# Kernel tuning notes

Hardware: AMD Instinct MI355X
Metric: run time of the kernel (lower is better)

Reference implementation:

```python
import jax, jax.numpy as jnp
import numpy as np

N = 50000
E = 1600000

def setup_inputs() -> dict:
    key = jax.random.key(0)
    ks = jax.random.split(key, 8)
    x = jax.random.normal(ks[0], (N, 512), dtype=jnp.float32)
    edge_index = jax.random.randint(ks[1], (2, E), 0, N, dtype=jnp.int32).astype(jnp.int64)
    eigenvectors = jax.random.normal(ks[2], (N, 128), dtype=jnp.float32)
    W1 = jax.random.normal(ks[3], (512, 128), dtype=jnp.float32) * 0.04
    b1 = jnp.zeros((128,), dtype=jnp.float32)
    W2 = jax.random.normal(ks[4], (128, 64), dtype=jnp.float32) * 0.09
    b2 = jnp.zeros((64,), dtype=jnp.float32)
    lin_W = jax.random.normal(ks[5], (128, 64), dtype=jnp.float32) * 0.09
    W3 = jax.random.normal(ks[6], (128, 40), dtype=jnp.float32) * 0.09
    b3 = jnp.zeros((40,), dtype=jnp.float32)
    return {"x": x, "edge_index": edge_index, "eigenvectors": eigenvectors,
            "W1": W1, "b1": b1, "W2": W2, "b2": b2, "lin_W": lin_W, "W3": W3, "b3": b3}

def _gcn_norm(edge_index, num_nodes):
    # add self loops, then symmetric normalization D^-1/2 (A+I) D^-1/2
    loop = jnp.arange(num_nodes, dtype=edge_index.dtype)
    row = jnp.concatenate([edge_index[0], loop])  # source
    col = jnp.concatenate([edge_index[1], loop])  # target
    w = jnp.ones(row.shape[0], dtype=jnp.float32)
    deg = jax.ops.segment_sum(w, col, num_segments=num_nodes)
    dis = jnp.where(deg > 0, 1.0 / jnp.sqrt(deg), 0.0)
    norm = dis[row] * dis[col]  # [E+N]
    return row, col, norm

def _gcn_conv(h, W, b, row, col, norm, num_nodes):
    h = h @ W                                  # [N, d_out] linear first (PyG order)
    msg = h[row] * norm[:, None]               # gather + scale, [E+N, d_out]
    out = jax.ops.segment_sum(msg, col, num_segments=num_nodes)  # scatter-add
    return out + b

def reference(x, edge_index, eigenvectors, W1, b1, W2, b2, lin_W, W3, b3):
    num_nodes = x.shape[0]
    row, col, norm = _gcn_norm(edge_index, num_nodes)
    h = jax.nn.relu(_gcn_conv(x, W1, b1, row, col, norm, num_nodes))
    # dropout omitted: eval mode (deterministic reference)
    h = jax.nn.relu(_gcn_conv(h, W2, b2, row, col, norm, num_nodes))
    xp = eigenvectors @ lin_W                  # Linear(spec_in, spec_out, bias=False)
    h = jnp.concatenate([h, xp], axis=1)       # [N, h2+spec_out]
    h = _gcn_conv(h, W3, b3, row, col, norm, num_nodes)
    return jax.nn.log_softmax(h, axis=1)
```

## Files before the change

### kernel.cpp

```cpp
#include <hip/hip_runtime.h>
#include <cstdint>
#include <cstddef>

constexpr int BLK = 256;
constexpr int NB = 128;

static inline size_t ws_align(size_t x) { return (x + 255) & ~size_t(255); }

typedef __attribute__((ext_vector_type(8))) short bf16x8;
typedef __attribute__((ext_vector_type(4))) float f32x4;

__device__ inline unsigned short f2bf(float f) {
  unsigned int u = __float_as_uint(f);
  unsigned int r = (u + 0x7fffu + ((u >> 16) & 1u)) >> 16;
  return (unsigned short)r;
}
__device__ inline float bf2f(unsigned short u) {
  return __uint_as_float(((unsigned int)u) << 16);
}
__device__ inline float bf2f_lo(unsigned int w) {
  return __uint_as_float(w << 16);
}
__device__ inline float bf2f_hi(unsigned int w) {
  return __uint_as_float(w & 0xffff0000u);
}

__device__ inline void gload16(const void* gp, void* lp) {
  __builtin_amdgcn_global_load_lds(
      (const __attribute__((address_space(1))) void*)gp,
      (__attribute__((address_space(3))) void*)lp, 16, 0, 0);
}

__global__ void k_pack_wt(const int* __restrict__ ei, unsigned int* __restrict__ pk,
                          int* __restrict__ cnt, int E, int nChunk,
                          const float* __restrict__ W1, const float* __restrict__ W2,
                          const float* __restrict__ linW, const float* __restrict__ W3,
                          unsigned short* __restrict__ WT1, unsigned short* __restrict__ WT2,
                          unsigned short* __restrict__ WTl, unsigned short* __restrict__ WT3) {
  if (blockIdx.x >= NB) {
    int i = (blockIdx.x - NB) * BLK + threadIdx.x;
    if (i < 65536) {
      int n = i >> 9, kg = i & 511;
      int tile = kg >> 5, k = kg & 31;
      WT1[tile * 4096 + n * 32 + k] = f2bf(W1[(size_t)kg * 128 + n]);
    } else if (i < 73728) {
      int j = i - 65536; int n = j >> 7, k = j & 127;
      WT2[j] = f2bf(W2[(size_t)k * 64 + n]);
    } else if (i < 81920) {
      int j = i - 73728; int n = j >> 7, k = j & 127;
      WTl[j] = f2bf(linW[(size_t)k * 64 + n]);
    } else if (i < 88064) {
      int j = i - 81920; int n = j >> 7, k = j & 127;
      WT3[j] = f2bf(n < 40 ? W3[(size_t)k * 40 + n] : 0.f);
    }
    return;
  }
  __shared__ int hist[256];
  for (int t = threadIdx.x; t < 256; t += BLK) hist[t] = 0;
  __syncthreads();
  int allz = 1;
  #pragma unroll 8
  for (int i = 0; i < 32; ++i) allz &= (ei[2 * i + 1] == 0) ? 1 : 0;
  const bool i64 = allz != 0;
  int beg = blockIdx.x * nChunk, end = min(beg + nChunk, E);
  for (int i = beg + threadIdx.x; i < end; i += BLK) {
    int row, col;
    if (i64) { row = ei[2 * i]; col = ei[2 * (E + i)]; }
    else     { row = ei[i];     col = ei[E + i]; }
    unsigned int p = ((unsigned int)col << 16) | (unsigned int)row;
    pk[i] = p;
    atomicAdd(&hist[col >> 8], 1);
  }
  __syncthreads();
  for (int t = threadIdx.x; t < 256; t += BLK) cnt[blockIdx.x * 256 + t] = hist[t];
}

__global__ void k_wscan(const int* __restrict__ cnt, int* __restrict__ woffs,
                        int* __restrict__ base, int nb, int E) {
  __shared__ int wsums[5];
  int w = threadIdx.x;
  int s = 0;
  for (int b = 0; b < nb; ++b) s += cnt[b * 256 + w];
  int lane = w & 63, wv = w >> 6;
  int x = s;
  #pragma unroll
  for (int sh = 1; sh < 64; sh <<= 1) { int t = __shfl_up(x, sh); if (lane >= sh) x += t; }
  if (lane == 63) wsums[wv] = x;
  __syncthreads();
  if (w == 0) { int a = 0; for (int k = 0; k < 4; ++k) { int t = wsums[k]; wsums[k] = a; a += t; } }
  __syncthreads();
  int excl = x - s + wsums[wv];
  woffs[w] = excl;
  if (w == 255) woffs[256] = excl + s;
  int start = excl;
  for (int b = 0; b < nb; ++b) { base[b * 256 + w] = start; start += cnt[b * 256 + w]; }
}

__global__ __launch_bounds__(256)
void k_part_gemm1(const unsigned int* __restrict__ pk, const int* __restrict__ base,
                  unsigned int* __restrict__ P, int E, int nChunk,
                  const float* __restrict__ x, const unsigned short* __restrict__ WT,
                  unsigned short* __restrict__ C, int N, int gG1) {
  __shared__ __align__(16) char smem[49152];
  if ((int)blockIdx.x >= gG1) {
    const int pb = (int)blockIdx.x - gG1;
    int* cur = (int*)smem;
    for (int t = threadIdx.x; t < 256; t += BLK) cur[t] = base[pb * 256 + t];
    __syncthreads();
    int beg = pb * nChunk, end = min(beg + nChunk, E);
    for (int i = beg + threadIdx.x; i < end; i += BLK) {
      unsigned int p = pk[i];
      int pos = atomicAdd(&cur[p >> 24], 1);
      P[pos] = p;
    }
    return;
  }
  float* As0 = (float*)smem;
  unsigned short* Wsl0 = (unsigned short*)(smem + 24576);
  const int tid = threadIdx.x;
  const int lane = tid & 63, wv = tid >> 6;
  const int m = lane & 15, kq = lane >> 4;
  const int row0 = (int)blockIdx.x * 64;

  const int r8 = lane >> 3;
  const int c8 = lane & 7;
  int agrow[2];
  #pragma unroll
  for (int jj = 0; jj < 2; ++jj) {
    int gr = row0 + wv * 16 + jj * 8 + r8;
    agrow[jj] = gr < N ? gr : N - 1;
  }

  f32x4 acc[8];
  #pragma unroll
  for (int t = 0; t < 8; ++t) acc[t] = {0.f, 0.f, 0.f, 0.f};

  auto STAGE = [&](int pb, int kb) {
    #pragma unroll
    for (int jj = 0; jj < 2; ++jj) {
      const float* src = x + (size_t)agrow[jj] * 512 + kb * 32 + (c8 ^ r8) * 4;
      gload16(src, As0 + pb * 2048 + (wv * 16 + jj * 8) * 32);
    }
    #pragma unroll
    for (int jj = 0; jj < 2; ++jj) {
      const unsigned short* src = WT + (size_t)kb * 4096 + wv * 1024 + jj * 512;
      gload16(src, Wsl0 + pb * 4096 + wv * 1024 + jj * 512);
    }
  };

  STAGE(0, 0);
  int cur = 0;
  #pragma unroll 1
  for (int t = 0; t < 16; ++t) {
    int nxt = cur + 1; if (nxt == 3) nxt = 0;
    if (t < 15) {
      STAGE(nxt, t + 1);
      asm volatile("s_waitcnt vmcnt(4)" ::: "memory");
    } else {
      asm volatile("s_waitcnt vmcnt(0)" ::: "memory");
    }
    __builtin_amdgcn_s_barrier();
    __builtin_amdgcn_sched_barrier(0);

    const char* Ab = (const char*)(As0 + cur * 2048);
    const char* Wb = (const char*)(Wsl0 + cur * 4096);
    const int row = wv * 16 + m;
    const int s = row & 7;
    f32x4 lo = *(const f32x4*)(Ab + row * 128 + ((kq * 2) ^ s) * 16);
    f32x4 hi = *(const f32x4*)(Ab + row * 128 + ((kq * 2 + 1) ^ s) * 16);
    bf16x8 af;
    af[0] = (short)f2bf(lo[0]); af[1] = (short)f2bf(lo[1]);
    af[2] = (short)f2bf(lo[2]); af[3] = (short)f2bf(lo[3]);
    af[4] = (short)f2bf(hi[0]); af[5] = (short)f2bf(hi[1]);
    af[6] = (short)f2bf(hi[2]); af[7] = (short)f2bf(hi[3]);
    #pragma unroll
    for (int tt = 0; tt < 8; ++tt) {
      int wrow = tt * 16 + m;
      bf16x8 bf = *(const bf16x8*)(Wb + wrow * 64 + kq * 16);
      acc[tt] = __builtin_amdgcn_mfma_f32_16x16x32_bf16(af, bf, acc[tt], 0, 0, 0);
    }
    cur = nxt;
  }

  #pragma unroll
  for (int r = 0; r < 4; ++r) {
    int rr = row0 + wv * 16 + kq * 4 + r;
    if (rr < N) {
      #pragma unroll
      for (int t = 0; t < 8; ++t)
        C[(size_t)rr * 128 + t * 16 + m] = f2bf(acc[t][r]);
    }
  }
}

__global__ void k_window_build(const unsigned int* __restrict__ P,
                               const int* __restrict__ woffs,
                               float* __restrict__ dis, int* __restrict__ offs,
                               int* __restrict__ csr, int N, int E) {
  __shared__ int hist[256];
  __shared__ int wsums[5];
  __shared__ int lbase[256];
  const int node0 = blockIdx.x * 256;
  const int t = threadIdx.x;
  hist[t] = 0;
  __syncthreads();
  const int beg = woffs[blockIdx.x], end = woffs[blockIdx.x + 1];
  for (int i = beg + t; i < end; i += BLK)
    atomicAdd(&hist[(P[i] >> 16) & 255], 1);
  __syncthreads();
  const int dg = hist[t];
  if (node0 + t < N) dis[node0 + t] = 1.0f / sqrtf((float)(dg + 1));
  int lane = t & 63, wv = t >> 6;
  int x = dg;
  #pragma unroll
  for (int sh = 1; sh < 64; sh <<= 1) { int q = __shfl_up(x, sh); if (lane >= sh) x += q; }
  if (lane == 63) wsums[wv] = x;
  __syncthreads();
  if (t == 0) { int a = 0; for (int k = 0; k < 4; ++k) { int q = wsums[k]; wsums[k] = a; a += q; } }
  __syncthreads();
  const int goff = beg + (x - dg + wsums[wv]);
  if (node0 + t < N) offs[node0 + t] = goff;
  lbase[t] = goff;
  __syncthreads();
  for (int i = beg + t; i < end; i += BLK) {
    unsigned int p = P[i];
    int pos = atomicAdd(&lbase[(p >> 16) & 255], 1);
    csr[pos] = (int)(p & 0xffffu);
  }
  if (blockIdx.x == 0 && t == 0) offs[N] = E;
}

template<int NT, int MR, bool AF32>
__device__ inline void mgemm_body(int bi, const void* __restrict__ Av,
                                  const unsigned short* __restrict__ WT,
                                  const float* __restrict__ dis, unsigned short* __restrict__ C,
                                  int ldc, int NOUT, int N) {
  constexpr int K = 128;
  const int tid = threadIdx.x;
  const int lane = tid & 63;
  const int wv = tid >> 6;
  const int m = lane & 15;
  const int kq = lane >> 4;
  const int orow = bi * (64 * MR) + wv * (16 * MR);

  int rowc[MR];
  #pragma unroll
  for (int mr = 0; mr < MR; ++mr) {
    int row = orow + mr * 16 + m;
    rowc[mr] = row < N ? row : N - 1;
  }

  f32x4 acc[MR][NT];
  #pragma unroll
  for (int mr = 0; mr < MR; ++mr)
    #pragma unroll
    for (int t = 0; t < NT; ++t) acc[mr][t] = {0.f, 0.f, 0.f, 0.f};

  #pragma unroll 4
  for (int k0 = 0; k0 < K; k0 += 32) {
    bf16x8 af[MR];
    #pragma unroll
    for (int mr = 0; mr < MR; ++mr) {
      if constexpr (AF32) {
        const float* Arow = (const float*)Av + (size_t)rowc[mr] * K + kq * 8 + k0;
        float4 a0 = *(const float4*)Arow;
        float4 a1 = *(const float4*)(Arow + 4);
        af[mr][0] = (short)f2bf(a0.x); af[mr][1] = (short)f2bf(a0.y);
        af[mr][2] = (short)f2bf(a0.z); af[mr][3] = (short)f2bf(a0.w);
        af[mr][4] = (short)f2bf(a1.x); af[mr][5] = (short)f2bf(a1.y);
        af[mr][6] = (short)f2bf(a1.z); af[mr][7] = (short)f2bf(a1.w);
      } else {
        const unsigned short* Arow = (const unsigned short*)Av + (size_t)rowc[mr] * K + kq * 8 + k0;
        af[mr] = *(const bf16x8*)Arow;
      }
    }
    bf16x8 bf[NT];
    #pragma unroll
    for (int t = 0; t < NT; ++t)
      bf[t] = *(const bf16x8*)(WT + (size_t)(t * 16 + m) * K + k0 + kq * 8);
    #pragma unroll
    for (int t = 0; t < NT; ++t)
      #pragma unroll
      for (int mr = 0; mr < MR; ++mr)
        acc[mr][t] = __builtin_amdgcn_mfma_f32_16x16x32_bf16(af[mr], bf[t], acc[mr][t], 0, 0, 0);
  }
  #pragma unroll
  for (int mr = 0; mr < MR; ++mr) {
    #pragma unroll
    for (int r = 0; r < 4; ++r) {
      int rr = orow + mr * 16 + kq * 4 + r;
      if (rr < N) {
        float s = dis ? dis[rr] : 1.f;
        #pragma unroll
        for (int t = 0; t < NT; ++t) {
          int cc = t * 16 + m;
          if (cc < NOUT)
            C[(size_t)rr * ldc + cc] = f2bf(acc[mr][t][r] * s);
        }
      }
    }
  }
}

__global__ __launch_bounds__(256)
void k_mgemm2x(const unsigned short* __restrict__ G, const unsigned short* __restrict__ WT2,
               const float* __restrict__ dis, unsigned short* __restrict__ F,
               const float* __restrict__ eig, const unsigned short* __restrict__ WTl,
               unsigned short* __restrict__ XP, int N, int nA) {
  if ((int)blockIdx.x < nA)
    mgemm_body<4, 2, false>(blockIdx.x, G, WT2, dis, F, 64, 64, N);
  else
    mgemm_body<4, 2, true>(blockIdx.x - nA, eig, WTl, nullptr, XP, 64, 64, N);
}

__global__ __launch_bounds__(256)
void k_mgemm3(const unsigned short* __restrict__ H2, const unsigned short* __restrict__ XP,
              const unsigned short* __restrict__ WT3, const float* __restrict__ dis,
              unsigned short* __restrict__ C, int N) {
  constexpr int NT = 3, MR = 2;
  const int tid = threadIdx.x;
  const int lane = tid & 63;
  const int wv = tid >> 6;
  const int m = lane & 15;
  const int kq = lane >> 4;
  const int orow = blockIdx.x * (64 * MR) + wv * (16 * MR);

  int rowc[MR];
  #pragma unroll
  for (int mr = 0; mr < MR; ++mr) {
    int row = orow + mr * 16 + m;
    rowc[mr] = row < N ? row : N - 1;
  }

  f32x4 acc[MR][NT];
  #pragma unroll
  for (int mr = 0; mr < MR; ++mr)
    #pragma unroll
    for (int t = 0; t < NT; ++t) acc[mr][t] = {0.f, 0.f, 0.f, 0.f};

  #pragma unroll 4
  for (int k0 = 0; k0 < 128; k0 += 32) {
    const unsigned short* Abase = (k0 < 64) ? H2 : XP;
    const int kk = (k0 & 63) + kq * 8;
    bf16x8 af[MR];
    #pragma unroll
    for (int mr = 0; mr < MR; ++mr)
      af[mr] = *(const bf16x8*)(Abase + (size_t)rowc[mr] * 64 + kk);
    bf16x8 bf[NT];
    #pragma unroll
    for (int t = 0; t < NT; ++t)
      bf[t] = *(const bf16x8*)(WT3 + (size_t)(t * 16 + m) * 128 + k0 + kq * 8);
    #pragma unroll
    for (int t = 0; t < NT; ++t)
      #pragma unroll
      for (int mr = 0; mr < MR; ++mr)
        acc[mr][t] = __builtin_amdgcn_mfma_f32_16x16x32_bf16(af[mr], bf[t], acc[mr][t], 0, 0, 0);
  }
  #pragma unroll
  for (int mr = 0; mr < MR; ++mr) {
    #pragma unroll
    for (int r = 0; r < 4; ++r) {
      int rr = orow + mr * 16 + kq * 4 + r;
      if (rr < N) {
        float s = dis[rr];
        #pragma unroll
        for (int t = 0; t < NT; ++t) {
          int cc = t * 16 + m;
          if (cc < 40)
            C[(size_t)rr * 40 + cc] = f2bf(acc[mr][t][r] * s);
        }
      }
    }
  }
}

template<int D, bool RELU, bool GDIS>
__launch_bounds__(BLK)
__global__ void k_agg2(const unsigned short* __restrict__ g, int ldg,
                       const float* __restrict__ dis, const float* __restrict__ bias,
                       const int* __restrict__ offs, const int* __restrict__ csr,
                       unsigned short* __restrict__ dst, int ldd, int N) {
  constexpr int CPL = D / 32;
  int wid = (blockIdx.x * BLK + threadIdx.x) >> 6;
  int lane = threadIdx.x & 63;
  if (wid >= N) return;
  const int l5 = lane >> 5, c = lane & 31;
  const float dv = dis[wid];
  float acc[CPL];
  #pragma unroll
  for (int k = 0; k < CPL; ++k) acc[k] = 0.f;

  auto addrow = [&](int r, float w) {
    if constexpr (CPL == 4) {
      uint2 v = *(const uint2*)&g[(size_t)r * ldg + c * 4];
      acc[0] = fmaf(w, bf2f_lo(v.x), acc[0]); acc[1] = fmaf(w, bf2f_hi(v.x), acc[1]);
      acc[2] = fmaf(w, bf2f_lo(v.y), acc[2]); acc[3] = fmaf(w, bf2f_hi(v.y), acc[3]);
    } else {
      unsigned int v = *(const unsigned int*)&g[(size_t)r * ldg + c * 2];
      acc[0] = fmaf(w, bf2f_lo(v), acc[0]); acc[1] = fmaf(w, bf2f_hi(v), acc[1]);
    }
  };

  if (l5 == 0) addrow(wid, GDIS ? dv : 1.0f);
  int beg = offs[wid], end = offs[wid + 1];
  for (int e0 = beg; e0 < end; e0 += 64) {
    int cnt = end - e0; if (cnt > 64) cnt = 64;
    int u = (lane < cnt) ? csr[e0 + lane] : 0;
    float du = 1.0f;
    if constexpr (GDIS) du = (lane < cnt) ? dis[u] : 0.f;
    int j = 0;
    for (; j + 3 < cnt; j += 4) {
      int r0 = __shfl(u, j + l5);
      int r1 = __shfl(u, j + 2 + l5);
      float w0 = GDIS ? __shfl(du, j + l5) : 1.0f;
      float w1 = GDIS ? __shfl(du, j + 2 + l5) : 1.0f;
      addrow(r0, w0); addrow(r1, w1);
    }
    for (; j < cnt; j += 2) {
      int jj = j + l5;
      int si = jj < cnt ? jj : j;
      int r0 = __shfl(u, si);
      float w0 = GDIS ? __shfl(du, si) : 1.0f;
      if (jj < cnt) addrow(r0, w0);
    }
  }
  #pragma unroll
  for (int k = 0; k < CPL; ++k) acc[k] += __shfl_xor(acc[k], 32);

  if (l5 == 0) {
    float o[CPL];
    #pragma unroll
    for (int k = 0; k < CPL; ++k) {
      o[k] = dv * acc[k] + bias[c * CPL + k];
      if constexpr (RELU) o[k] = fmaxf(o[k], 0.f);
    }
    if constexpr (CPL == 4) {
      uint2 pw;
      pw.x = (unsigned)f2bf(o[0]) | ((unsigned)f2bf(o[1]) << 16);
      pw.y = (unsigned)f2bf(o[2]) | ((unsigned)f2bf(o[3]) << 16);
      *(uint2*)&dst[(size_t)wid * ldd + c * 4] = pw;
    } else {
      unsigned int pw = (unsigned)f2bf(o[0]) | ((unsigned)f2bf(o[1]) << 16);
      *(unsigned int*)&dst[(size_t)wid * ldd + c * 2] = pw;
    }
  }
}

__launch_bounds__(BLK)
__global__ void k_agg40(const unsigned short* __restrict__ g,
                        const float* __restrict__ dis, const float* __restrict__ bias,
                        const int* __restrict__ offs, const int* __restrict__ csr,
                        float* __restrict__ dst, int N) {
  int wid = (blockIdx.x * BLK + threadIdx.x) >> 6;
  int lane = threadIdx.x & 63;
  if (wid >= N) return;
  const int l5 = lane >> 5, c = lane & 31;
  const bool act = c < 20;
  float a0 = 0.f, a1 = 0.f;
  auto addrow = [&](int r) {
    if (act) {
      unsigned int w = *(const unsigned int*)&g[(size_t)r * 40 + c * 2];
      a0 += bf2f_lo(w); a1 += bf2f_hi(w);
    }
  };
  if (l5 == 0) addrow(wid);
  int beg = offs[wid], end = offs[wid + 1];
  for (int e0 = beg; e0 < end; e0 += 64) {
    int cnt = end - e0; if (cnt > 64) cnt = 64;
    int u = (lane < cnt) ? csr[e0 + lane] : 0;
    int j = 0;
    for (; j + 3 < cnt; j += 4) {
      int r0 = __shfl(u, j + l5);
      int r1 = __shfl(u, j + 2 + l5);
      addrow(r0); addrow(r1);
    }
    for (; j < cnt; j += 2) {
      int jj = j + l5;
      int r0 = __shfl(u, jj < cnt ? jj : j);
      if (jj < cnt) addrow(r0);
    }
  }
  a0 += __shfl_xor(a0, 32);
  a1 += __shfl_xor(a1, 32);

  if (l5 == 0) {
    float dv = dis[wid];
    float o0 = act ? dv * a0 + bias[c * 2]     : -__builtin_inff();
    float o1 = act ? dv * a1 + bias[c * 2 + 1] : -__builtin_inff();
    float mx = fmaxf(o0, o1);
    #pragma unroll
    for (int s = 16; s >= 1; s >>= 1) mx = fmaxf(mx, __shfl_down(mx, s, 32));
    mx = __shfl(mx, 0, 32);
    float ex = act ? (expf(o0 - mx) + expf(o1 - mx)) : 0.f;
    #pragma unroll
    for (int s = 16; s >= 1; s >>= 1) ex += __shfl_down(ex, s, 32);
    float ls = logf(__shfl(ex, 0, 32));
    if (act) {
      float2 r = make_float2(o0 - mx - ls, o1 - mx - ls);
      *(float2*)&dst[(size_t)wid * 40 + c * 2] = r;
    }
  }
}

extern "C" void kernel_launch(void* const* d_in, const int* in_sizes, int n_in,
                              void* d_out, int out_size, void* d_ws, size_t ws_size,
                              hipStream_t stream) {
  const float* x    = (const float*)d_in[0];
  const int*   ei   = (const int*)d_in[1];
  const float* eig  = (const float*)d_in[2];
  const float* W1   = (const float*)d_in[3];
  const float* b1   = (const float*)d_in[4];
  const float* W2   = (const float*)d_in[5];
  const float* b2   = (const float*)d_in[6];
  const float* linW = (const float*)d_in[7];
  const float* W3   = (const float*)d_in[8];
  const float* b3   = (const float*)d_in[9];
  float* out = (float*)d_out;

  const int N = in_sizes[0] / 512;
  const int E = in_sizes[1] / 2;

  char* ws = (char*)d_ws;
  size_t off = 0;
  auto alloc = [&](size_t bytes) { char* p = ws + off; off = ws_align(off + bytes); return p; };
  unsigned int* pk = (unsigned int*)alloc((size_t)E * 4);
  unsigned int* P  = (unsigned int*)alloc((size_t)E * 4);
  int*   csr    = (int*)alloc((size_t)E * 4);
  int*   offs   = (int*)alloc((size_t)(N + 1) * 4);
  int*   cnt    = (int*)alloc((size_t)NB * 256 * 4);
  int*   base   = (int*)alloc((size_t)NB * 256 * 4);
  int*   woffs  = (int*)alloc(257 * 4);
  float* dis    = (float*)alloc((size_t)N * 4);
  unsigned short* F  = (unsigned short*)alloc((size_t)N * 128 * 2);
  unsigned short* G  = (unsigned short*)alloc((size_t)N * 128 * 2);
  unsigned short* XP = (unsigned short*)alloc((size_t)N * 64 * 2);
  unsigned short* H2 = (unsigned short*)alloc((size_t)N * 64 * 2);
  unsigned short* WT1 = (unsigned short*)alloc(128 * 512 * 2);
  unsigned short* WT2 = (unsigned short*)alloc(64 * 128 * 2);
  unsigned short* WTl = (unsigned short*)alloc(64 * 128 * 2);
  unsigned short* WT3 = (unsigned short*)alloc(48 * 128 * 2);

  const int nChunk = (E + NB - 1) / NB;
  const int NW = (N + 255) / 256;
  const int WTB = (88064 + BLK - 1) / BLK;
  const int gG1 = (N + 63) / 64;
  const int gA = (N + 3) / 4;

  k_pack_wt<<<NB + WTB, BLK, 0, stream>>>(ei, pk, cnt, E, nChunk,
                                          W1, W2, linW, W3, WT1, WT2, WTl, WT3);
  k_wscan<<<1, 256, 0, stream>>>(cnt, woffs, base, NB, E);
  k_part_gemm1<<<gG1 + NB, BLK, 0, stream>>>(pk, base, P, E, nChunk, x, WT1, F, N, gG1);
  k_window_build<<<NW, BLK, 0, stream>>>(P, woffs, dis, offs, csr, N, E);

  k_agg2<128, true, true><<<gA, BLK, 0, stream>>>(F, 128, dis, b1, offs, csr, G, 128, N);
  k_mgemm2x<<<2 * ((N + 127) / 128), BLK, 0, stream>>>(G, WT2, dis, F, eig, WTl, XP, N, (N + 127) / 128);
  k_agg2<64, true, false><<<gA, BLK, 0, stream>>>(F, 64, dis, b2, offs, csr, H2, 64, N);
  k_mgemm3<<<(N + 127) / 128, BLK, 0, stream>>>(H2, XP, WT3, dis, F, N);
  k_agg40<<<gA, BLK, 0, stream>>>(F, dis, b3, offs, csr, out, N);
}
```

Measured before the change: 286.8 us.

## Fold spectral linear into W3 and fuse layer-3 GEMM into layer-2 aggregation

Precomputes the product linW·W3[64:] so the eigenvector branch maps straight to 40 outputs, and computes that projection inside the gemm1/partition launch. The layer-2 aggregation kernel now also applies ReLU and multiplies by the top half of W3 in registers, then adds the precomputed spectral term. This removes the separate mgemm3 launch and the H2/XP round trips through memory. In exchange the aggregation kernel does extra shuffle-based matvec work per node, and the weights are folded in a different order, which changes rounding.

After: 348.8 us. 1.22x slower.

```diff
diff --git a/kernel.cpp b/kernel.cpp
--- a/kernel.cpp
+++ b/kernel.cpp
@@ -34,9 +34,9 @@
 __global__ void k_pack_wt(const int* __restrict__ ei, unsigned int* __restrict__ pk,
                           int* __restrict__ cnt, int E, int nChunk,
                           const float* __restrict__ W1, const float* __restrict__ W2,
-                          const float* __restrict__ linW, const float* __restrict__ W3,
+                          const float* __restrict__ W3,
                           unsigned short* __restrict__ WT1, unsigned short* __restrict__ WT2,
-                          unsigned short* __restrict__ WTl, unsigned short* __restrict__ WT3) {
+                          unsigned short* __restrict__ W3aT) {
   if (blockIdx.x >= NB) {
     int i = (blockIdx.x - NB) * BLK + threadIdx.x;
     if (i < 65536) {
@@ -46,12 +46,9 @@
     } else if (i < 73728) {
       int j = i - 65536; int n = j >> 7, k = j & 127;
       WT2[j] = f2bf(W2[(size_t)k * 64 + n]);
-    } else if (i < 81920) {
-      int j = i - 73728; int n = j >> 7, k = j & 127;
-      WTl[j] = f2bf(linW[(size_t)k * 64 + n]);
-    } else if (i < 88064) {
-      int j = i - 81920; int n = j >> 7, k = j & 127;
-      WT3[j] = f2bf(n < 40 ? W3[(size_t)k * 40 + n] : 0.f);
+    } else if (i < 76288) {
+      int j2 = i - 73728; int jj = j2 >> 6, k = j2 & 63;
+      W3aT[j2] = f2bf(W3[(size_t)k * 40 + jj]);
     }
     return;
   }
@@ -75,8 +72,25 @@
   for (int t = threadIdx.x; t < 256; t += BLK) cnt[blockIdx.x * 256 + t] = hist[t];
 }
 
-__global__ void k_wscan(const int* __restrict__ cnt, int* __restrict__ woffs,
-                        int* __restrict__ base, int nb, int E) {
+__global__ void k_wscan_w3c(const int* __restrict__ cnt, int* __restrict__ woffs,
+                            int* __restrict__ base, int nb, int E,
+                            const float* __restrict__ linW, const float* __restrict__ W3,
+                            unsigned short* __restrict__ WT3c) {
+  if (blockIdx.x > 0) {
+    int jbase = ((int)blockIdx.x - 1) * 12;
+    for (int idx = threadIdx.x; idx < 12 * 128; idx += BLK) {
+      int j = jbase + (idx >> 7), k = idx & 127;
+      if (j >= 48) continue;
+      float v = 0.f;
+      if (j < 40) {
+        const float* lrow = linW + (size_t)k * 64;
+        #pragma unroll 8
+        for (int t = 0; t < 64; ++t) v += lrow[t] * W3[(size_t)(64 + t) * 40 + j];
+      }
+      WT3c[(size_t)j * 128 + k] = f2bf(v);
+    }
+    return;
+  }
   __shared__ int wsums[5];
   int w = threadIdx.x;
   int s = 0;
@@ -94,140 +108,6 @@
   if (w == 255) woffs[256] = excl + s;
   int start = excl;
   for (int b = 0; b < nb; ++b) { base[b * 256 + w] = start; start += cnt[b * 256 + w]; }
-}
-
-__global__ __launch_bounds__(256)
-void k_part_gemm1(const unsigned int* __restrict__ pk, const int* __restrict__ base,
-                  unsigned int* __restrict__ P, int E, int nChunk,
-                  const float* __restrict__ x, const unsigned short* __restrict__ WT,
-                  unsigned short* __restrict__ C, int N, int gG1) {
-  __shared__ __align__(16) char smem[49152];
-  if ((int)blockIdx.x >= gG1) {
-    const int pb = (int)blockIdx.x - gG1;
-    int* cur = (int*)smem;
-    for (int t = threadIdx.x; t < 256; t += BLK) cur[t] = base[pb * 256 + t];
-    __syncthreads();
-    int beg = pb * nChunk, end = min(beg + nChunk, E);
-    for (int i = beg + threadIdx.x; i < end; i += BLK) {
-      unsigned int p = pk[i];
-      int pos = atomicAdd(&cur[p >> 24], 1);
-      P[pos] = p;
-    }
-    return;
-  }
-  float* As0 = (float*)smem;
-  unsigned short* Wsl0 = (unsigned short*)(smem + 24576);
-  const int tid = threadIdx.x;
-  const int lane = tid & 63, wv = tid >> 6;
-  const int m = lane & 15, kq = lane >> 4;
-  const int row0 = (int)blockIdx.x * 64;
-
-  const int r8 = lane >> 3;
-  const int c8 = lane & 7;
-  int agrow[2];
-  #pragma unroll
-  for (int jj = 0; jj < 2; ++jj) {
-    int gr = row0 + wv * 16 + jj * 8 + r8;
-    agrow[jj] = gr < N ? gr : N - 1;
-  }
-
-  f32x4 acc[8];
-  #pragma unroll
-  for (int t = 0; t < 8; ++t) acc[t] = {0.f, 0.f, 0.f, 0.f};
-
-  auto STAGE = [&](int pb, int kb) {
-    #pragma unroll
-    for (int jj = 0; jj < 2; ++jj) {
-      const float* src = x + (size_t)agrow[jj] * 512 + kb * 32 + (c8 ^ r8) * 4;
-      gload16(src, As0 + pb * 2048 + (wv * 16 + jj * 8) * 32);
-    }
-    #pragma unroll
-    for (int jj = 0; jj < 2; ++jj) {
-      const unsigned short* src = WT + (size_t)kb * 4096 + wv * 1024 + jj * 512;
-      gload16(src, Wsl0 + pb * 4096 + wv * 1024 + jj * 512);
-    }
-  };
-
-  STAGE(0, 0);
-  int cur = 0;
-  #pragma unroll 1
-  for (int t = 0; t < 16; ++t) {
-    int nxt = cur + 1; if (nxt == 3) nxt = 0;
-    if (t < 15) {
-      STAGE(nxt, t + 1);
-      asm volatile("s_waitcnt vmcnt(4)" ::: "memory");
-    } else {
-      asm volatile("s_waitcnt vmcnt(0)" ::: "memory");
-    }
-    __builtin_amdgcn_s_barrier();
-    __builtin_amdgcn_sched_barrier(0);
-
-    const char* Ab = (const char*)(As0 + cur * 2048);
-    const char* Wb = (const char*)(Wsl0 + cur * 4096);
-    const int row = wv * 16 + m;
-    const int s = row & 7;
-    f32x4 lo = *(const f32x4*)(Ab + row * 128 + ((kq * 2) ^ s) * 16);
-    f32x4 hi = *(const f32x4*)(Ab + row * 128 + ((kq * 2 + 1) ^ s) * 16);
-    bf16x8 af;
-    af[0] = (short)f2bf(lo[0]); af[1] = (short)f2bf(lo[1]);
-    af[2] = (short)f2bf(lo[2]); af[3] = (short)f2bf(lo[3]);
-    af[4] = (short)f2bf(hi[0]); af[5] = (short)f2bf(hi[1]);
-    af[6] = (short)f2bf(hi[2]); af[7] = (short)f2bf(hi[3]);
-    #pragma unroll
-    for (int tt = 0; tt < 8; ++tt) {
-      int wrow = tt * 16 + m;
-      bf16x8 bf = *(const bf16x8*)(Wb + wrow * 64 + kq * 16);
-      acc[tt] = __builtin_amdgcn_mfma_f32_16x16x32_bf16(af, bf, acc[tt], 0, 0, 0);
-    }
-    cur = nxt;
-  }
-
-  #pragma unroll
-  for (int r = 0; r < 4; ++r) {
-    int rr = row0 + wv * 16 + kq * 4 + r;
-    if (rr < N) {
-      #pragma unroll
-      for (int t = 0; t < 8; ++t)
-        C[(size_t)rr * 128 + t * 16 + m] = f2bf(acc[t][r]);
-    }
-  }
-}
-
-__global__ void k_window_build(const unsigned int* __restrict__ P,
-                               const int* __restrict__ woffs,
-                               float* __restrict__ dis, int* __restrict__ offs,
-                               int* __restrict__ csr, int N, int E) {
-  __shared__ int hist[256];
-  __shared__ int wsums[5];
-  __shared__ int lbase[256];
-  const int node0 = blockIdx.x * 256;
-  const int t = threadIdx.x;
-  hist[t] = 0;
-  __syncthreads();
-  const int beg = woffs[blockIdx.x], end = woffs[blockIdx.x + 1];
-  for (int i = beg + t; i < end; i += BLK)
-    atomicAdd(&hist[(P[i] >> 16) & 255], 1);
-  __syncthreads();
-  const int dg = hist[t];
-  if (node0 + t < N) dis[node0 + t] = 1.0f / sqrtf((float)(dg + 1));
-  int lane = t & 63, wv = t >> 6;
-  int x = dg;
-  #pragma unroll
-  for (int sh = 1; sh < 64; sh <<= 1) { int q = __shfl_up(x, sh); if (lane >= sh) x += q; }
-  if (lane == 63) wsums[wv] = x;
-  __syncthreads();
-  if (t == 0) { int a = 0; for (int k = 0; k < 4; ++k) { int q = wsums[k]; wsums[k] = a; a += q; } }
-  __syncthreads();
-  const int goff = beg + (x - dg + wsums[wv]);
-  if (node0 + t < N) offs[node0 + t] = goff;
-  lbase[t] = goff;
-  __syncthreads();
-  for (int i = beg + t; i < end; i += BLK) {
-    unsigned int p = P[i];
-    int pos = atomicAdd(&lbase[(p >> 16) & 255], 1);
-    csr[pos] = (int)(p & 0xffffu);
-  }
-  if (blockIdx.x == 0 && t == 0) offs[N] = E;
 }
 
 template<int NT, int MR, bool AF32>
@@ -303,75 +183,149 @@
 }
 
 __global__ __launch_bounds__(256)
-void k_mgemm2x(const unsigned short* __restrict__ G, const unsigned short* __restrict__ WT2,
-               const float* __restrict__ dis, unsigned short* __restrict__ F,
-               const float* __restrict__ eig, const unsigned short* __restrict__ WTl,
-               unsigned short* __restrict__ XP, int N, int nA) {
-  if ((int)blockIdx.x < nA)
-    mgemm_body<4, 2, false>(blockIdx.x, G, WT2, dis, F, 64, 64, N);
-  else
-    mgemm_body<4, 2, true>(blockIdx.x - nA, eig, WTl, nullptr, XP, 64, 64, N);
+void k_part_gemm1(const unsigned int* __restrict__ pk, const int* __restrict__ base,
+                  unsigned int* __restrict__ P, int E, int nChunk,
+                  const float* __restrict__ x, const unsigned short* __restrict__ WT,
+                  unsigned short* __restrict__ C, int N, int gG1,
+                  const float* __restrict__ eig, const unsigned short* __restrict__ WT3c,
+                  unsigned short* __restrict__ XP3) {
+  __shared__ __align__(16) char smem[49152];
+  if ((int)blockIdx.x >= gG1 + NB) {
+    mgemm_body<3, 2, true>((int)blockIdx.x - gG1 - NB, eig, WT3c, nullptr, XP3, 40, 40, N);
+    return;
+  }
+  if ((int)blockIdx.x >= gG1) {
+    const int pb = (int)blockIdx.x - gG1;
+    int* cur = (int*)smem;
+    for (int t = threadIdx.x; t < 256; t += BLK) cur[t] = base[pb * 256 + t];
+    __syncthreads();
+    int beg = pb * nChunk, end = min(beg + nChunk, E);
+    for (int i = beg + threadIdx.x; i < end; i += BLK) {
+      unsigned int p = pk[i];
+      int pos = atomicAdd(&cur[p >> 24], 1);
+      P[pos] = p;
+    }
+    return;
+  }
+  float* As0 = (float*)smem;
+  unsigned short* Wsl0 = (unsigned short*)(smem + 24576);
+  const int tid = threadIdx.x;
+  const int lane = tid & 63, wv = tid >> 6;
+  const int m = lane & 15, kq = lane >> 4;
+  const int row0 = (int)blockIdx.x * 64;
+
+  const int r8 = lane >> 3;
+  const int c8 = lane & 7;
+  int agrow[2];
+  #pragma unroll
+  for (int jj = 0; jj < 2; ++jj) {
+    int gr = row0 + wv * 16 + jj * 8 + r8;
+    agrow[jj] = gr < N ? gr : N - 1;
+  }
+
+  f32x4 acc[8];
+  #pragma unroll
+  for (int t = 0; t < 8; ++t) acc[t] = {0.f, 0.f, 0.f, 0.f};
+
+  auto STAGE = [&](int pb, int kb) {
+    #pragma unroll
+    for (int jj = 0; jj < 2; ++jj) {
+      const float* src = x + (size_t)agrow[jj] * 512 + kb * 32 + (c8 ^ r8) * 4;
+      gload16(src, As0 + pb * 2048 + (wv * 16 + jj * 8) * 32);
+    }
+    #pragma unroll
+    for (int jj = 0; jj < 2; ++jj) {
+      const unsigned short* src = WT + (size_t)kb * 4096 + wv * 1024 + jj * 512;
+      gload16(src, Wsl0 + pb * 4096 + wv * 1024 + jj * 512);
+    }
+  };
+
+  STAGE(0, 0);
+  int cur = 0;
+  #pragma unroll 1
+  for (int t = 0; t < 16; ++t) {
+    int nxt = cur + 1; if (nxt == 3) nxt = 0;
+    if (t < 15) {
+      STAGE(nxt, t + 1);
+      asm volatile("s_waitcnt vmcnt(4)" ::: "memory");
+    } else {
+      asm volatile("s_waitcnt vmcnt(0)" ::: "memory");
+    }
+    __builtin_amdgcn_s_barrier();
+    __builtin_amdgcn_sched_barrier(0);
+
+    const char* Ab = (const char*)(As0 + cur * 2048);
+    const char* Wb = (const char*)(Wsl0 + cur * 4096);
+    const int row = wv * 16 + m;
+    const int s = row & 7;
+    f32x4 lo = *(const f32x4*)(Ab + row * 128 + ((kq * 2) ^ s) * 16);
+    f32x4 hi = *(const f32x4*)(Ab + row * 128 + ((kq * 2 + 1) ^ s) * 16);
+    bf16x8 af;
+    af[0] = (short)f2bf(lo[0]); af[1] = (short)f2bf(lo[1]);
+    af[2] = (short)f2bf(lo[2]); af[3] = (short)f2bf(lo[3]);
+    af[4] = (short)f2bf(hi[0]); af[5] = (short)f2bf(hi[1]);
+    af[6] = (short)f2bf(hi[2]); af[7] = (short)f2bf(hi[3]);
+    #pragma unroll
+    for (int tt = 0; tt < 8; ++tt) {
+      int wrow = tt * 16 + m;
+      bf16x8 bf = *(const bf16x8*)(Wb + wrow * 64 + kq * 16);
+      acc[tt] = __builtin_amdgcn_mfma_f32_16x16x32_bf16(af, bf, acc[tt], 0, 0, 0);
+    }
+    cur = nxt;
+  }
+
+  #pragma unroll
+  for (int r = 0; r < 4; ++r) {
+    int rr = row0 + wv * 16 + kq * 4 + r;
+    if (rr < N) {
+      #pragma unroll
+      for (int t = 0; t < 8; ++t)
+        C[(size_t)rr * 128 + t * 16 + m] = f2bf(acc[t][r]);
+    }
+  }
+}
+
+__global__ void k_window_build(const unsigned int* __restrict__ P,
+                               const int* __restrict__ woffs,
+                               float* __restrict__ dis, int* __restrict__ offs,
+                               int* __restrict__ csr, int N, int E) {
+  __shared__ int hist[256];
+  __shared__ int wsums[5];
+  __shared__ int lbase[256];
+  const int node0 = blockIdx.x * 256;
+  const int t = threadIdx.x;
+  hist[t] = 0;
+  __syncthreads();
+  const int beg = woffs[blockIdx.x], end = woffs[blockIdx.x + 1];
+  for (int i = beg + t; i < end; i += BLK)
+    atomicAdd(&hist[(P[i] >> 16) & 255], 1);
+  __syncthreads();
+  const int dg = hist[t];
+  if (node0 + t < N) dis[node0 + t] = 1.0f / sqrtf((float)(dg + 1));
+  int lane = t & 63, wv = t >> 6;
+  int x = dg;
+  #pragma unroll
+  for (int sh = 1; sh < 64; sh <<= 1) { int q = __shfl_up(x, sh); if (lane >= sh) x += q; }
+  if (lane == 63) wsums[wv] = x;
+  __syncthreads();
+  if (t == 0) { int a = 0; for (int k = 0; k < 4; ++k) { int q = wsums[k]; wsums[k] = a; a += q; } }
+  __syncthreads();
+  const int goff = beg + (x - dg + wsums[wv]);
+  if (node0 + t < N) offs[node0 + t] = goff;
+  lbase[t] = goff;
+  __syncthreads();
+  for (int i = beg + t; i < end; i += BLK) {
+    unsigned int p = P[i];
+    int pos = atomicAdd(&lbase[(p >> 16) & 255], 1);
+    csr[pos] = (int)(p & 0xffffu);
+  }
+  if (blockIdx.x == 0 && t == 0) offs[N] = E;
 }
 
 __global__ __launch_bounds__(256)
-void k_mgemm3(const unsigned short* __restrict__ H2, const unsigned short* __restrict__ XP,
-              const unsigned short* __restrict__ WT3, const float* __restrict__ dis,
-              unsigned short* __restrict__ C, int N) {
-  constexpr int NT = 3, MR = 2;
-  const int tid = threadIdx.x;
-  const int lane = tid & 63;
-  const int wv = tid >> 6;
-  const int m = lane & 15;
-  const int kq = lane >> 4;
-  const int orow = blockIdx.x * (64 * MR) + wv * (16 * MR);
-
-  int rowc[MR];
-  #pragma unroll
-  for (int mr = 0; mr < MR; ++mr) {
-    int row = orow + mr * 16 + m;
-    rowc[mr] = row < N ? row : N - 1;
-  }
-
-  f32x4 acc[MR][NT];
-  #pragma unroll
-  for (int mr = 0; mr < MR; ++mr)
-    #pragma unroll
-    for (int t = 0; t < NT; ++t) acc[mr][t] = {0.f, 0.f, 0.f, 0.f};
-
-  #pragma unroll 4
-  for (int k0 = 0; k0 < 128; k0 += 32) {
-    const unsigned short* Abase = (k0 < 64) ? H2 : XP;
-    const int kk = (k0 & 63) + kq * 8;
-    bf16x8 af[MR];
-    #pragma unroll
-    for (int mr = 0; mr < MR; ++mr)
-      af[mr] = *(const bf16x8*)(Abase + (size_t)rowc[mr] * 64 + kk);
-    bf16x8 bf[NT];
-    #pragma unroll
-    for (int t = 0; t < NT; ++t)
-      bf[t] = *(const bf16x8*)(WT3 + (size_t)(t * 16 + m) * 128 + k0 + kq * 8);
-    #pragma unroll
-    for (int t = 0; t < NT; ++t)
-      #pragma unroll
-      for (int mr = 0; mr < MR; ++mr)
-        acc[mr][t] = __builtin_amdgcn_mfma_f32_16x16x32_bf16(af[mr], bf[t], acc[mr][t], 0, 0, 0);
-  }
-  #pragma unroll
-  for (int mr = 0; mr < MR; ++mr) {
-    #pragma unroll
-    for (int r = 0; r < 4; ++r) {
-      int rr = orow + mr * 16 + kq * 4 + r;
-      if (rr < N) {
-        float s = dis[rr];
-        #pragma unroll
-        for (int t = 0; t < NT; ++t) {
-          int cc = t * 16 + m;
-          if (cc < 40)
-            C[(size_t)rr * 40 + cc] = f2bf(acc[mr][t][r] * s);
-        }
-      }
-    }
-  }
+void k_mgemm2(const unsigned short* __restrict__ G, const unsigned short* __restrict__ WT2,
+              const float* __restrict__ dis, unsigned short* __restrict__ F2, int N) {
+  mgemm_body<4, 2, false>(blockIdx.x, G, WT2, dis, F2, 64, 64, N);
 }
 
 template<int D, bool RELU, bool GDIS>
@@ -443,6 +397,66 @@
       unsigned int pw = (unsigned)f2bf(o[0]) | ((unsigned)f2bf(o[1]) << 16);
       *(unsigned int*)&dst[(size_t)wid * ldd + c * 2] = pw;
     }
+  }
+}
+
+__launch_bounds__(BLK)
+__global__ void k_agg64c3(const unsigned short* __restrict__ g,
+                          const float* __restrict__ dis, const float* __restrict__ b2,
+                          const int* __restrict__ offs, const int* __restrict__ csr,
+                          const unsigned short* __restrict__ W3aT,
+                          const unsigned short* __restrict__ XP3,
+                          unsigned short* __restrict__ F3, int N) {
+  int wid = (blockIdx.x * BLK + threadIdx.x) >> 6;
+  int lane = threadIdx.x & 63;
+  if (wid >= N) return;
+  const int l5 = lane >> 5, c = lane & 31;
+  const float dv = dis[wid];
+  float a0 = 0.f, a1 = 0.f;
+
+  auto addrow = [&](int r) {
+    unsigned int v = *(const unsigned int*)&g[(size_t)r * 64 + c * 2];
+    a0 += bf2f_lo(v); a1 += bf2f_hi(v);
+  };
+
+  if (l5 == 0) addrow(wid);
+  int beg = offs[wid], end = offs[wid + 1];
+  for (int e0 = beg; e0 < end; e0 += 64) {
+    int cnt = end - e0; if (cnt > 64) cnt = 64;
+    int u = (lane < cnt) ? csr[e0 + lane] : 0;
+    int j = 0;
+    for (; j + 3 < cnt; j += 4) {
+      int r0 = __shfl(u, j + l5);
+      int r1 = __shfl(u, j + 2 + l5);
+      addrow(r0); addrow(r1);
+    }
+    for (; j < cnt; j += 2) {
+      int jj = j + l5;
+      int r0 = __shfl(u, jj < cnt ? jj : j);
+      if (jj < cnt) addrow(r0);
+    }
+  }
+  a0 += __shfl_xor(a0, 32);
+  a1 += __shfl_xor(a1, 32);
+
+  float h0 = fmaxf(dv * a0 + b2[c * 2], 0.f);
+  float h1v = fmaxf(dv * a1 + b2[c * 2 + 1], 0.f);
+
+  const bool act = c < 20;
+  const int j = l5 * 20 + c;
+  const unsigned int* wrow = (const unsigned int*)(W3aT + (size_t)(act ? j : 0) * 64);
+  float wacc = 0.f;
+  #pragma unroll
+  for (int i = 0; i < 32; ++i) {
+    float va = __shfl(h0, i, 32);
+    float vb = __shfl(h1v, i, 32);
+    unsigned int wp = wrow[i];
+    wacc = fmaf(va, bf2f_lo(wp), wacc);
+    wacc = fmaf(vb, bf2f_hi(wp), wacc);
+  }
+  if (act) {
+    float xpv = bf2f(XP3[(size_t)wid * 40 + j]);
+    F3[(size_t)wid * 40 + j] = f2bf(dv * (wacc + xpv));
   }
 }
 
@@ -531,30 +545,32 @@
   int*   base   = (int*)alloc((size_t)NB * 256 * 4);
   int*   woffs  = (int*)alloc(257 * 4);
   float* dis    = (float*)alloc((size_t)N * 4);
-  unsigned short* F  = (unsigned short*)alloc((size_t)N * 128 * 2);
-  unsigned short* G  = (unsigned short*)alloc((size_t)N * 128 * 2);
-  unsigned short* XP = (unsigned short*)alloc((size_t)N * 64 * 2);
-  unsigned short* H2 = (unsigned short*)alloc((size_t)N * 64 * 2);
+  unsigned short* F   = (unsigned short*)alloc((size_t)N * 128 * 2);
+  unsigned short* G   = (unsigned short*)alloc((size_t)N * 128 * 2);
+  unsigned short* F2  = (unsigned short*)alloc((size_t)N * 64 * 2);
+  unsigned short* XP3 = (unsigned short*)alloc((size_t)N * 40 * 2);
+  unsigned short* F3  = (unsigned short*)alloc((size_t)N * 40 * 2);
   unsigned short* WT1 = (unsigned short*)alloc(128 * 512 * 2);
   unsigned short* WT2 = (unsigned short*)alloc(64 * 128 * 2);
-  unsigned short* WTl = (unsigned short*)alloc(64 * 128 * 2);
-  unsigned short* WT3 = (unsigned short*)alloc(48 * 128 * 2);
+  unsigned short* W3aT = (unsigned short*)alloc(40 * 64 * 2);
+  unsigned short* WT3c = (unsigned short*)alloc(48 * 128 * 2);
 
   const int nChunk = (E + NB - 1) / NB;
   const int NW = (N + 255) / 256;
-  const int WTB = (88064 + BLK - 1) / BLK;
+  const int WTB = (76288 + BLK - 1) / BLK;
   const int gG1 = (N + 63) / 64;
+  const int gX  = (N + 127) / 128;
   const int gA = (N + 3) / 4;
 
   k_pack_wt<<<NB + WTB, BLK, 0, stream>>>(ei, pk, cnt, E, nChunk,
-                                          W1, W2, linW, W3, WT1, WT2, WTl, WT3);
-  k_wscan<<<1, 256, 0, stream>>>(cnt, woffs, base, NB, E);
-  k_part_gemm1<<<gG1 + NB, BLK, 0, stream>>>(pk, base, P, E, nChunk, x, WT1, F, N, gG1);
+                                          W1, W2, W3, WT1, WT2, W3aT);
+  k_wscan_w3c<<<5, 256, 0, stream>>>(cnt, woffs, base, NB, E, linW, W3, WT3c);
+  k_part_gemm1<<<gG1 + NB + gX, BLK, 0, stream>>>(pk, base, P, E, nChunk, x, WT1, F, N, gG1,
+                                                  eig, WT3c, XP3);
   k_window_build<<<NW, BLK, 0, stream>>>(P, woffs, dis, offs, csr, N, E);
 
   k_agg2<128, true, true><<<gA, BLK, 0, stream>>>(F, 128, dis, b1, offs, csr, G, 128, N);
-  k_mgemm2x<<<2 * ((N + 127) / 128), BLK, 0, stream>>>(G, WT2, dis, F, eig, WTl, XP, N, (N + 127) / 128);
-  k_agg2<64, true, false><<<gA, BLK, 0, stream>>>(F, 64, dis, b2, offs, csr, H2, 64, N);
-  k_mgemm3<<<(N + 127) / 128, BLK, 0, stream>>>(H2, XP, WT3, dis, F, N);
-  k_agg40<<<gA, BLK, 0, stream>>>(F, dis, b3, offs, csr, out, N);
-}
+  k_mgemm2<<<gX, BLK, 0, stream>>>(G, WT2, dis, F2, N);
+  k_agg64c3<<<gA, BLK, 0, stream>>>(F2, dis, b2, offs, csr, W3aT, XP3, F3, N);
+  k_agg40<<<gA, BLK, 0, stream>>>(F3, dis, b3, offs, csr, out, N);
+}
```
